# Kernel tuning notes

Measured on AMD Instinct MI355X. Metric: run time of the kernel, lower is better.

## Reference

```python
import jax, jax.numpy as jnp
import numpy as np

H = 16  # num_heads
B, N, M, D = 4, 512, 2048, 1024
FF = 4096  # mlp_ratio * D
LN_EPS = 1e-5


def _ln(x, g, b):
    m = x.mean(-1, keepdims=True)
    v = ((x - m) ** 2).mean(-1, keepdims=True)
    return (x - m) * jax.lax.rsqrt(v + LN_EPS) * g + b


def _attn(q_in, k_in, v_in, wq, bq, wk, bk, wv, bv, wp, bp):
    b, n, d = q_in.shape
    m = k_in.shape[1]
    hd = d // H
    scale = hd ** -0.5
    q = (q_in @ wq + bq).reshape(b, n, H, hd) * scale
    k = (k_in @ wk + bk).reshape(b, m, H, hd)
    v = (v_in @ wv + bv).reshape(b, m, H, hd)
    attn = jax.nn.softmax(jnp.einsum('bnhd,bmhd->bhnm', q, k), axis=-1)
    out = jnp.einsum('bhnm,bmhd->bnhd', attn, v).reshape(b, n, d)
    return out @ wp + bp


def setup_inputs() -> dict:
    key = jax.random.key(0)
    ks = iter(jax.random.split(key, 32))
    rnd = lambda shape: jax.random.normal(next(ks), shape, dtype=jnp.float32)
    w = lambda *shape: rnd(shape) * 0.02
    inp = {
        'state': rnd((B, N, D)),
        'patches': rnd((B, M, D)),
        'patches_pos_embed': rnd((B, M, D)),
        'state_query': rnd((B, N, D)),
    }
    for p in ('ca', 'sa'):
        inp[f'{p}_wq'] = w(D, D); inp[f'{p}_bq'] = jnp.zeros((D,), jnp.float32)
        inp[f'{p}_wk'] = w(D, D); inp[f'{p}_bk'] = jnp.zeros((D,), jnp.float32)
        inp[f'{p}_wv'] = w(D, D); inp[f'{p}_bv'] = jnp.zeros((D,), jnp.float32)
        inp[f'{p}_wp'] = w(D, D); inp[f'{p}_bp'] = jnp.zeros((D,), jnp.float32)
    inp['w1'] = w(D, FF); inp['b1'] = jnp.zeros((FF,), jnp.float32)
    inp['w2'] = w(FF, D); inp['b2'] = jnp.zeros((D,), jnp.float32)
    for i in (1, 2, 3):
        inp[f'n{i}_g'] = jnp.ones((D,), jnp.float32)
        inp[f'n{i}_b'] = jnp.zeros((D,), jnp.float32)
        inp[f'ls{i}'] = jnp.full((D,), 1e-5, jnp.float32)
    return inp


def reference(state, patches, patches_pos_embed, state_query,
              ca_wq, ca_bq, ca_wk, ca_bk, ca_wv, ca_bv, ca_wp, ca_bp,
              sa_wq, sa_bq, sa_wk, sa_bk, sa_wv, sa_bv, sa_wp, sa_bp,
              w1, b1, w2, b2,
              n1_g, n1_b, n2_g, n2_b, n3_g, n3_b,
              ls1, ls2, ls3):
    # pre-norm path of TransformerLayer.forward_pre (dropouts/drop_path = 0)
    state = state + state_query
    kv = patches + patches_pos_embed
    cross = _attn(_ln(state, n1_g, n1_b), kv, patches,
                  ca_wq, ca_bq, ca_wk, ca_bk, ca_wv, ca_bv, ca_wp, ca_bp)
    state = state + cross * ls1
    ns = _ln(state, n2_g, n2_b)
    selfa = _attn(ns, ns, ns,
                  sa_wq, sa_bq, sa_wk, sa_bk, sa_wv, sa_bv, sa_wp, sa_bp)
    state = state + selfa * ls2
    h = jax.nn.gelu(_ln(state, n3_g, n3_b) @ w1 + b1)
    return state + (h @ w2 + b2) * ls3
```

## Files before the change

### kernel.cpp

```cpp
#include <hip/hip_runtime.h>

#define DEV __device__ __forceinline__

typedef __bf16 bf16x8 __attribute__((ext_vector_type(8)));
typedef float f32x4 __attribute__((ext_vector_type(4)));

DEV unsigned short f2bf(float f) {
  __bf16 h = (__bf16)f;
  return __builtin_bit_cast(unsigned short, h);
}
DEV unsigned int cvtpk(float lo, float hi) {
  unsigned int r;
  asm("v_cvt_pk_bf16_f32 %0, %1, %2" : "=v"(r) : "v"(lo), "v"(hi));
  return r;
}

DEV void gload16(const void* g, void* l) {
  __builtin_amdgcn_global_load_lds(
      (const __attribute__((address_space(1))) unsigned int*)g,
      (__attribute__((address_space(3))) unsigned int*)l, 16, 0, 0);
}

DEV float gelu(float v) {
  const float u = 0.7978845608028654f * (v + 0.044715f * v * v * v);
  const float e = exp2f(u * 2.885390081777927f);
  return 0.5f * v * (2.f - 2.f / (e + 1.f));
}

DEV void tconv64_body(const float* __restrict__ W, unsigned short* __restrict__ Wt,
                      int K, int N, int bx, int by, float* tile ) {
  const int t = threadIdx.x;
  const int rr = t >> 4;
  const int cc = (t & 15) * 4;
#pragma unroll
  for (int it = 0; it < 4; it++) {
    float4 v = *reinterpret_cast<const float4*>(
        &W[(size_t)(by * 64 + it * 16 + rr) * N + bx * 64 + cc]);
    tile[(it * 16 + rr) * 65 + cc] = v.x;
    tile[(it * 16 + rr) * 65 + cc + 1] = v.y;
    tile[(it * 16 + rr) * 65 + cc + 2] = v.z;
    tile[(it * 16 + rr) * 65 + cc + 3] = v.w;
  }
  __syncthreads();
  const int nr = t >> 3;
  const int kc = (t & 7) * 8;
#pragma unroll
  for (int it = 0; it < 2; it++) {
    const int n = it * 32 + nr;
    uint4 o;
    o.x = cvtpk(tile[(kc + 0) * 65 + n], tile[(kc + 1) * 65 + n]);
    o.y = cvtpk(tile[(kc + 2) * 65 + n], tile[(kc + 3) * 65 + n]);
    o.z = cvtpk(tile[(kc + 4) * 65 + n], tile[(kc + 5) * 65 + n]);
    o.w = cvtpk(tile[(kc + 6) * 65 + n], tile[(kc + 7) * 65 + n]);
    *reinterpret_cast<uint4*>(&Wt[(size_t)(bx * 64 + n) * K + by * 64 + kc]) = o;
  }
}

DEV void add_ln_body(const float* __restrict__ a, const float* b, float* x0_out,
                     unsigned short* __restrict__ y, const float* __restrict__ gam,
                     const float* __restrict__ bet, int row) {
  const int t = threadIdx.x;
  const int c = t * 4;
  const size_t base = (size_t)row * 1024 + c;
  float4 v = *reinterpret_cast<const float4*>(a + base);
  if (b) {
    float4 v2 = *reinterpret_cast<const float4*>(b + base);
    v.x += v2.x; v.y += v2.y; v.z += v2.z; v.w += v2.w;
  }
  if (x0_out) *reinterpret_cast<float4*>(x0_out + base) = v;
  float s = v.x + v.y + v.z + v.w;
  float sq = v.x * v.x + v.y * v.y + v.z * v.z + v.w * v.w;
#pragma unroll
  for (int o = 32; o > 0; o >>= 1) {
    s += __shfl_xor(s, o);
    sq += __shfl_xor(sq, o);
  }
  __shared__ float ps[4], pq[4];
  const int w = t >> 6;
  if ((t & 63) == 0) { ps[w] = s; pq[w] = sq; }
  __syncthreads();
  s = ps[0] + ps[1] + ps[2] + ps[3];
  sq = pq[0] + pq[1] + pq[2] + pq[3];
  const float mean = s * (1.f / 1024.f);
  const float var = sq * (1.f / 1024.f) - mean * mean;
  const float rstd = rsqrtf(var + 1e-5f);
  float4 gv = *reinterpret_cast<const float4*>(gam + c);
  float4 bv = *reinterpret_cast<const float4*>(bet + c);
  uint2 o2;
  o2.x = cvtpk((v.x - mean) * rstd * gv.x + bv.x, (v.y - mean) * rstd * gv.y + bv.y);
  o2.y = cvtpk((v.z - mean) * rstd * gv.z + bv.z, (v.w - mean) * rstd * gv.w + bv.w);
  *reinterpret_cast<uint2*>(y + base) = o2;
}

DEV void kvcast_body8(const float* __restrict__ p, const float* __restrict__ pe,
                      unsigned short* __restrict__ kvo, unsigned short* __restrict__ po,
                      int bid) {
  const size_t i = ((size_t)bid * 256 + threadIdx.x) * 8;
  float4 a0 = *reinterpret_cast<const float4*>(p + i);
  float4 a1 = *reinterpret_cast<const float4*>(p + i + 4);
  float4 b0 = *reinterpret_cast<const float4*>(pe + i);
  float4 b1 = *reinterpret_cast<const float4*>(pe + i + 4);
  uint4 kv, pp;
  kv.x = cvtpk(a0.x + b0.x, a0.y + b0.y);
  kv.y = cvtpk(a0.z + b0.z, a0.w + b0.w);
  kv.z = cvtpk(a1.x + b1.x, a1.y + b1.y);
  kv.w = cvtpk(a1.z + b1.z, a1.w + b1.w);
  pp.x = cvtpk(a0.x, a0.y);
  pp.y = cvtpk(a0.z, a0.w);
  pp.z = cvtpk(a1.x, a1.y);
  pp.w = cvtpk(a1.z, a1.w);
  *reinterpret_cast<uint4*>(kvo + i) = kv;
  *reinterpret_cast<uint4*>(po + i) = pp;
}

struct Pre {
  const float* caw[3]; unsigned short* cad[3];
  const float* state; const float* squery; float* stateF; unsigned short* lnB;
  const float* n1_g; const float* n1_b;
  const float* patches; const float* ppe; unsigned short* kvB; unsigned short* patB;
};
__global__ __launch_bounds__(256) void prelude_kernel(Pre p) {
  __shared__ __align__(16) float tile[64 * 65];
  const int bid = blockIdx.x;
  if (bid < 4096) {
    kvcast_body8(p.patches, p.ppe, p.kvB, p.patB, bid);
  } else if (bid < 4864) {
    const int i = bid - 4096;
    const int m = i >> 8, wi = i & 255;
    tconv64_body(p.caw[m], p.cad[m], 1024, 1024, wi & 15, wi >> 4, tile);
  } else {
    add_ln_body(p.state, p.squery, p.stateF, p.lnB, p.n1_g, p.n1_b, bid - 4864);
  }
}

__global__ __launch_bounds__(256) void add_ln_kernel(
    const float* __restrict__ a, const float* b, float* x0_out,
    unsigned short* __restrict__ y, const float* __restrict__ gam,
    const float* __restrict__ bet) {
  add_ln_body(a, b, x0_out, y, gam, bet, blockIdx.x);
}

DEV void xcd_swizzle(int gx, int gy, int& bx, int& by, int& bz) {
  const int gxy = gx * gy;
  const int nwg = gxy * gridDim.z;
  const int orig = (blockIdx.z * gy + blockIdx.y) * gx + blockIdx.x;
  const int q = nwg >> 3, r = nwg & 7;
  const int xcd = orig & 7;
  int wgid = (xcd < r ? xcd * (q + 1) : r * (q + 1) + (xcd - r) * q) + (orig >> 3);
  bz = wgid / gxy;
  wgid -= bz * gxy;
  if (gy >= gx) { by = wgid / gx; bx = wgid - by * gx; }
  else          { bx = wgid / gy; by = wgid - bx * gy; }
}

template <int BM, int BN>
DEV void gemm_core(const unsigned short* __restrict__ A,
                   const unsigned short* __restrict__ Bt,
                   unsigned short* As, unsigned short* Bs,
                   int brow, int bcol, int K, int lda, int koff,
                   f32x4 (&acc)[BM / 32][BN / 32]) {
  constexpr int WM = BM / 32, WN = BN / 32;
  const int t = threadIdx.x;
  const int lane = t & 63, w = t >> 6;
  const int wr = w >> 1, wc = w & 1;
  const int g = lane >> 4, lr = lane & 15;
  const int srow = lane >> 2, scol = (lane & 3) * 8;

  auto stage = [&](int buf, int k0) {
#pragma unroll
    for (int i = 0; i < BM / 64; i++) {
      const int r0 = (i * 4 + w) * 16;
      gload16(A + (size_t)(brow + r0 + srow) * lda + koff + k0 + scol,
              &As[buf * BM * 32 + r0 * 32]);
    }
#pragma unroll
    for (int i = 0; i < BN / 64; i++) {
      const int r0 = (i * 4 + w) * 16;
      gload16(Bt + (size_t)(bcol + r0 + srow) * lda + koff + k0 + scol,
              &Bs[buf * BN * 32 + r0 * 32]);
    }
  };

  stage(0, 0);
  const int nk = K / 32;
  int cur = 0;
  for (int kt = 0; kt < nk; kt++) {
    __syncthreads();
    if (kt + 1 < nk) stage(cur ^ 1, (kt + 1) * 32);
    bf16x8 af[WM], bfr[WN];
#pragma unroll
    for (int m = 0; m < WM; m++)
      af[m] = *reinterpret_cast<const bf16x8*>(
          &As[cur * BM * 32 + (wr * (BM / 2) + m * 16 + lr) * 32 + g * 8]);
#pragma unroll
    for (int n = 0; n < WN; n++)
      bfr[n] = *reinterpret_cast<const bf16x8*>(
          &Bs[cur * BN * 32 + (wc * (BN / 2) + n * 16 + lr) * 32 + g * 8]);
    __builtin_amdgcn_s_setprio(1);
#pragma unroll
    for (int m = 0; m < WM; m++)
#pragma unroll
      for (int n = 0; n < WN; n++)
        acc[m][n] = __builtin_amdgcn_mfma_f32_16x16x32_bf16(af[m], bfr[n], acc[m][n], 0, 0, 0);
    __builtin_amdgcn_s_setprio(0);
    cur ^= 1;
  }
}

template <int BM, int BN>
DEV void epilogue_vT(f32x4 (&acc)[BM / 32][BN / 32], unsigned short* smem,
                     unsigned short* __restrict__ vT, const float* __restrict__ bias,
                     int brow, int bcol, int vcol0, int vNk, int rpb) {
  constexpr int WM = BM / 32, WN = BN / 32;
  constexpr int LDT = 136;
  const int t = threadIdx.x, lane = t & 63, w = t >> 6;
  const int wr = w >> 1, wc = w & 1;
  const int g = lane >> 4, lr = lane & 15;
  __syncthreads();
#pragma unroll
  for (int m = 0; m < WM; m++) {
    const int row0 = wr * (BM / 2) + m * 16 + g * 4;
#pragma unroll
    for (int n = 0; n < WN; n++) {
      const int cc = wc * (BN / 2) + n * 16 + lr;
      const float bv = bias[bcol + cc];
      uint2 pk;
      pk.x = cvtpk(acc[m][n][0] + bv, acc[m][n][1] + bv);
      pk.y = cvtpk(acc[m][n][2] + bv, acc[m][n][3] + bv);
      *reinterpret_cast<uint2*>(&smem[cc * LDT + row0]) = pk;
    }
  }
  __syncthreads();
  const int b = brow / rpb;
  const int kvb = brow % rpb;
  constexpr int ITERS = BM * BN / (256 * 8);
#pragma unroll
  for (int it = 0; it < ITERS; it++) {
    const int idx = it * 256 + t;
    const int cc = idx / (BM / 8);
    const int ch = idx % (BM / 8);
    const int dg = bcol + cc - vcol0;
    const int h = dg >> 6, d = dg & 63;
    uint4 v = *reinterpret_cast<uint4*>(&smem[cc * LDT + ch * 8]);
    *reinterpret_cast<uint4*>(
        &vT[((size_t)(b * 16 + h) * 64 + d) * vNk + kvb + ch * 8]) = v;
  }
}

template <int EPI, int BM, int BN>
__global__ __launch_bounds__(256) void gemm_kernel(
    const unsigned short* __restrict__ A, const unsigned short* __restrict__ Bt,
    const float* __restrict__ bias, const float* resid,
    const float* __restrict__ ls, void* outp, int M, int N, int K, int lda) {
  constexpr int WM = BM / 32;
  constexpr int WN = BN / 32;
  __shared__ __align__(16) unsigned short smem[2 * BM * 32 + 2 * BN * 32];
  unsigned short* As = smem;
  unsigned short* Bs = smem + 2 * BM * 32;
  const int t = threadIdx.x;
  const int lane = t & 63, w = t >> 6;
  const int wr = w >> 1, wc = w & 1;
  const int g = lane >> 4, lr = lane & 15;

  int bx, by, bz;
  xcd_swizzle(gridDim.x, gridDim.y, bx, by, bz);
  const int brow = by * BM, bcol = bx * BN;

  f32x4 acc[WM][WN] = {};
  gemm_core<BM, BN>(A, Bt, As, Bs, brow, bcol, K, lda, bz * K, acc);

#pragma unroll
  for (int m = 0; m < WM; m++) {
    const int row0 = brow + wr * (BM / 2) + m * 16 + g * 4;
#pragma unroll
    for (int n = 0; n < WN; n++) {
      const int col = bcol + wc * (BN / 2) + n * 16 + lr;
      const float bv = (EPI == 4) ? 0.f : bias[col];
#pragma unroll
      for (int r = 0; r < 4; r++) {
        const float v = acc[m][n][r] + bv;
        const size_t idx = (size_t)(row0 + r) * N + col;
        if (EPI == 0) {
          ((unsigned short*)outp)[idx] = f2bf(v);
        } else if (EPI == 2) {
          ((float*)outp)[idx] = resid[idx] + v * ls[col];
        } else if (EPI == 3) {
          ((unsigned short*)outp)[idx] = f2bf(gelu(v));
        } else {
          ((float*)outp)[(size_t)bz * M * N + idx] = v;
        }
      }
    }
  }
}

struct G3X {
  const unsigned short* A[3]; const unsigned short* Bt[3];
  const float* bias[3]; unsigned short* out[3]; int ecum[3];
  unsigned short* vT; int vNk; int rpb;
  const float* wp; unsigned short* wpt;
  const float* saw[4]; unsigned short* sad[4];
  const float* bq; const float* bk; const float* bv; float* bqkv;
};
__global__ __launch_bounds__(256) void gemm3_kernel(G3X p, int N, int K) {
  constexpr int BM = 128, BN = 128, WM = BM / 32, WN = BN / 32;
  constexpr int STG = 2 * BM * 32 + 2 * BN * 32;
  constexpr int TRN = BN * 136;
  constexpr int SME = (TRN > STG) ? TRN : STG;
  constexpr int NG = 1152;
  __shared__ __align__(16) unsigned short smem[SME];
  const int bid = blockIdx.x;
  const int t = threadIdx.x;

  if (bid >= NG) {
    float* tile = reinterpret_cast<float*>(smem);
    int i = bid - NG;
    if (i < 256) {
      tconv64_body(p.wp, p.wpt, 1024, 1024, i & 15, i >> 4, tile);
    } else if (i < 1280) {
      i -= 256;
      const int m = i >> 8, wi = i & 255;
      tconv64_body(p.saw[m], p.sad[m], 1024, 1024, wi & 15, wi >> 4, tile);
    } else {
      const int j = (i - 1280) * 256 + t;
      p.bqkv[j] = j < 1024 ? p.bq[j] : (j < 2048 ? p.bk[j - 1024] : p.bv[j - 2048]);
    }
    return;
  }

  unsigned short* As = smem;
  unsigned short* Bs = smem + 2 * BM * 32;
  const int lane = t & 63, w = t >> 6;
  const int wr = w >> 1, wc = w & 1;
  const int g = lane >> 4, lr = lane & 15;
  const int wgid = (bid & 7) * (NG >> 3) + (bid >> 3);
  const int by = wgid >> 3, bx = wgid & 7;
  const int s = (by >= p.ecum[0]) + (by >= p.ecum[1]);
  const int byloc = by - (s ? p.ecum[s - 1] : 0);
  const unsigned short* A = p.A[s];
  const unsigned short* Bt = p.Bt[s];
  const float* bias = p.bias[s];
  const int brow = byloc * BM, bcol = bx * BN;

  f32x4 acc[WM][WN] = {};
  gemm_core<BM, BN>(A, Bt, As, Bs, brow, bcol, K, K, 0, acc);

  if (s == 2) {
    epilogue_vT<BM, BN>(acc, smem, p.vT, bias, brow, bcol, 0, p.vNk, p.rpb);
    return;
  }
  unsigned short* outp = p.out[s];
#pragma unroll
  for (int m = 0; m < WM; m++) {
    const int row0 = brow + wr * (BM / 2) + m * 16 + g * 4;
#pragma unroll
    for (int n = 0; n < WN; n++) {
      const int col = bcol + wc * (BN / 2) + n * 16 + lr;
      const float bv = bias[col];
#pragma unroll
      for (int r = 0; r < 4; r++)
        outp[(size_t)(row0 + r) * N + col] = f2bf(acc[m][n][r] + bv);
    }
  }
}

struct G5X {
  const unsigned short* A; const unsigned short* Bt;
  const float* bias; unsigned short* out;
  unsigned short* vT; int vcol0; int vNk; int rpb;
  const float* w1; unsigned short* w1t;
  const float* w2; unsigned short* w2t;
};
__global__ __launch_bounds__(256) void gemm5x_kernel(G5X p, int M, int N, int K) {
  constexpr int BM = 128, BN = 64, WM = BM / 32, WN = BN / 32;
  constexpr int STG = 2 * BM * 32 + 2 * BN * 32;
  __shared__ __align__(16) unsigned short smem[STG];
  constexpr int NG = 768;
  const int bid = blockIdx.x;
  const int t = threadIdx.x;

  if (bid >= NG) {
    float* tile = reinterpret_cast<float*>(smem);
    int i = bid - NG;
    if (i < 1024) {
      tconv64_body(p.w1, p.w1t, 1024, 4096, i & 63, i >> 6, tile);
    } else {
      i -= 1024;
      tconv64_body(p.w2, p.w2t, 4096, 1024, i & 15, i >> 4, tile);
    }
    return;
  }

  unsigned short* As = smem;
  unsigned short* Bs = smem + 2 * BM * 32;
  const int lane = t & 63, w = t >> 6;
  const int wr = w >> 1, wc = w & 1;
  const int g = lane >> 4, lr = lane & 15;
  const int wgid = (bid & 7) * (NG >> 3) + (bid >> 3);
  const int bx = wgid >> 4, by = wgid & 15;
  const int brow = by * BM, bcol = bx * BN;

  f32x4 acc[WM][WN] = {};
  gemm_core<BM, BN>(p.A, p.Bt, As, Bs, brow, bcol, K, K, 0, acc);

  if (bcol >= p.vcol0) {
    epilogue_vT<BM, BN>(acc, smem, p.vT, p.bias, brow, bcol, p.vcol0, p.vNk, p.rpb);
    return;
  }
#pragma unroll
  for (int m = 0; m < WM; m++) {
    const int row0 = brow + wr * (BM / 2) + m * 16 + g * 4;
#pragma unroll
    for (int n = 0; n < WN; n++) {
      const int col = bcol + wc * (BN / 2) + n * 16 + lr;
      const float bv = p.bias[col];
#pragma unroll
      for (int r = 0; r < 4; r++)
        p.out[(size_t)(row0 + r) * N + col] = f2bf(acc[m][n][r] + bv);
    }
  }
}

__global__ __launch_bounds__(256) void splitk_red_kernel(
    const float* __restrict__ p, const float* __restrict__ bias,
    const float* __restrict__ resid, const float* __restrict__ ls,
    float* __restrict__ out) {
  const size_t i = ((size_t)blockIdx.x * 256 + threadIdx.x) * 4;
  const int c = (int)(i & 1023);
  float4 a = *reinterpret_cast<const float4*>(p + i);
  float4 b = *reinterpret_cast<const float4*>(p + 2048ull * 1024 + i);
  float4 rv = *reinterpret_cast<const float4*>(resid + i);
  float4 bb = *reinterpret_cast<const float4*>(bias + c);
  float4 lv = *reinterpret_cast<const float4*>(ls + c);
  float4 o;
  o.x = rv.x + (a.x + b.x + bb.x) * lv.x;
  o.y = rv.y + (a.y + b.y + bb.y) * lv.y;
  o.z = rv.z + (a.z + b.z + bb.z) * lv.z;
  o.w = rv.w + (a.w + b.w + bb.w) * lv.w;
  *reinterpret_cast<float4*>(out + i) = o;
}

__global__ __launch_bounds__(512) void attn_kernel(
    const unsigned short* __restrict__ Q, const unsigned short* __restrict__ Kp,
    const unsigned short* __restrict__ vT, unsigned short* __restrict__ O,
    int RSq, int RSk, int Nq, int Nk, float k2) {
  __shared__ __align__(16) unsigned short Ks[2][128 * 72];
  __shared__ __align__(16) unsigned short Vs[2][64 * 136];
  __shared__ __align__(16) unsigned short Ps[128 * 136];
  const int t = threadIdx.x, lane = t & 63, w = t >> 6;
  const int qt = blockIdx.y, h = blockIdx.x & 15, b = blockIdx.x >> 4;
  const int g = lane >> 4, lr = lane & 15;
  const int ksrow = t >> 2, kscol = (t & 3) * 16;
  const int vsrow = t >> 3, vscol = (t & 7) * 16;

  uint4 qr[2];
  {
    const unsigned short* qp = Q + (size_t)(b * Nq + qt * 128 + w * 16 + lr) * RSq + h * 64 + g * 8;
    qr[0] = *reinterpret_cast<const uint4*>(qp);
    qr[1] = *reinterpret_cast<const uint4*>(qp + 32);
  }
  float m_i = -1e30f, l_i = 0.f;
  f32x4 acc_o[4] = {};

  auto kaddr = [&](int kv0) {
    return reinterpret_cast<const uint4*>(
        Kp + (size_t)(b * Nk + kv0 + ksrow) * RSk + h * 64 + kscol);
  };
  auto vaddr = [&](int kv0) {
    return reinterpret_cast<const uint4*>(
        vT + ((size_t)(b * 16 + h) * 64 + vsrow) * Nk + kv0 + vscol);
  };

  uint4 kr0 = kaddr(0)[0], kr1 = kaddr(0)[1];
  uint4 vr0 = vaddr(0)[0], vr1 = vaddr(0)[1];

  int cur = 0;
  for (int kv0 = 0; kv0 < Nk; kv0 += 128) {
    *reinterpret_cast<uint4*>(&Ks[cur][ksrow * 72 + kscol]) = kr0;
    *reinterpret_cast<uint4*>(&Ks[cur][ksrow * 72 + kscol + 8]) = kr1;
    *reinterpret_cast<uint4*>(&Vs[cur][vsrow * 136 + vscol]) = vr0;
    *reinterpret_cast<uint4*>(&Vs[cur][vsrow * 136 + vscol + 8]) = vr1;
    __syncthreads();
    if (kv0 + 128 < Nk) {
      kr0 = kaddr(kv0 + 128)[0]; kr1 = kaddr(kv0 + 128)[1];
      vr0 = vaddr(kv0 + 128)[0]; vr1 = vaddr(kv0 + 128)[1];
    }

    f32x4 accs[8] = {};
    __builtin_amdgcn_s_setprio(1);
#pragma unroll
    for (int d0 = 0; d0 < 64; d0 += 32) {
      bf16x8 qf = __builtin_bit_cast(bf16x8, qr[d0 >> 5]);
#pragma unroll
      for (int m = 0; m < 8; m++) {
        bf16x8 kf = *reinterpret_cast<const bf16x8*>(&Ks[cur][(m * 16 + lr) * 72 + d0 + g * 8]);
        accs[m] = __builtin_amdgcn_mfma_f32_16x16x32_bf16(kf, qf, accs[m], 0, 0, 0);
      }
    }
    __builtin_amdgcn_s_setprio(0);
    float pmax = -1e30f;
#pragma unroll
    for (int m = 0; m < 8; m++)
#pragma unroll
      for (int r = 0; r < 4; r++) pmax = fmaxf(pmax, accs[m][r]);
    pmax = fmaxf(pmax, __shfl_xor(pmax, 16));
    pmax = fmaxf(pmax, __shfl_xor(pmax, 32));
    const float pm2 = pmax * k2;
    if (!__all(pm2 <= m_i + 8.f)) {
      const float m_new = fmaxf(m_i, pm2);
      const float corr = exp2f(m_i - m_new);
      m_i = m_new;
      l_i *= corr;
#pragma unroll
      for (int r = 0; r < 4; r++) {
        const float cf = __shfl(corr, g * 4 + r);
#pragma unroll
        for (int n = 0; n < 4; n++) acc_o[n][r] *= cf;
      }
    }
    float psum = 0.f;
#pragma unroll
    for (int m = 0; m < 8; m++) {
      float p0 = exp2f(fmaf(accs[m][0], k2, -m_i));
      float p1 = exp2f(fmaf(accs[m][1], k2, -m_i));
      float p2 = exp2f(fmaf(accs[m][2], k2, -m_i));
      float p3 = exp2f(fmaf(accs[m][3], k2, -m_i));
      psum += p0 + p1 + p2 + p3;
      uint2 pk;
      pk.x = cvtpk(p0, p1);
      pk.y = cvtpk(p2, p3);
      *reinterpret_cast<uint2*>(&Ps[(w * 16 + lr) * 136 + m * 16 + g * 4]) = pk;
    }
    psum += __shfl_xor(psum, 16);
    psum += __shfl_xor(psum, 32);
    l_i += psum;
    __builtin_amdgcn_s_setprio(1);
#pragma unroll
    for (int ks = 0; ks < 4; ks++) {
      bf16x8 pf = *reinterpret_cast<const bf16x8*>(&Ps[(w * 16 + lr) * 136 + ks * 32 + g * 8]);
#pragma unroll
      for (int n = 0; n < 4; n++) {
        bf16x8 vf = *reinterpret_cast<const bf16x8*>(&Vs[cur][(n * 16 + lr) * 136 + ks * 32 + g * 8]);
        acc_o[n] = __builtin_amdgcn_mfma_f32_16x16x32_bf16(pf, vf, acc_o[n], 0, 0, 0);
      }
    }
    __builtin_amdgcn_s_setprio(0);
    cur ^= 1;
  }
#pragma unroll
  for (int r = 0; r < 4; r++) {
    const float li = __shfl(l_i, g * 4 + r);
    const float inv = 1.f / li;
    const int qrow = qt * 128 + w * 16 + g * 4 + r;
#pragma unroll
    for (int n = 0; n < 4; n++)
      O[(size_t)(b * Nq + qrow) * 1024 + h * 64 + n * 16 + lr] = f2bf(acc_o[n][r] * inv);
  }
}

extern "C" void kernel_launch(void* const* d_in, const int* in_sizes, int n_in,
                              void* d_out, int out_size, void* d_ws, size_t ws_size,
                              hipStream_t stream) {
  const float* state = (const float*)d_in[0];
  const float* patches = (const float*)d_in[1];
  const float* ppe = (const float*)d_in[2];
  const float* squery = (const float*)d_in[3];
  const float* ca_wq = (const float*)d_in[4];
  const float* ca_bq = (const float*)d_in[5];
  const float* ca_wk = (const float*)d_in[6];
  const float* ca_bk = (const float*)d_in[7];
  const float* ca_wv = (const float*)d_in[8];
  const float* ca_bv = (const float*)d_in[9];
  const float* ca_wp = (const float*)d_in[10];
  const float* ca_bp = (const float*)d_in[11];
  const float* sa_wq = (const float*)d_in[12];
  const float* sa_bq = (const float*)d_in[13];
  const float* sa_wk = (const float*)d_in[14];
  const float* sa_bk = (const float*)d_in[15];
  const float* sa_wv = (const float*)d_in[16];
  const float* sa_bv = (const float*)d_in[17];
  const float* sa_wp = (const float*)d_in[18];
  const float* sa_bp = (const float*)d_in[19];
  const float* w1 = (const float*)d_in[20];
  const float* b1 = (const float*)d_in[21];
  const float* w2 = (const float*)d_in[22];
  const float* b2 = (const float*)d_in[23];
  const float* n1_g = (const float*)d_in[24];
  const float* n1_b = (const float*)d_in[25];
  const float* ls1 = (const float*)d_in[26];
  const float* n2_g = (const float*)d_in[27];
  const float* n2_b = (const float*)d_in[28];
  const float* ls2 = (const float*)d_in[29];
  const float* n3_g = (const float*)d_in[30];
  const float* n3_b = (const float*)d_in[31];
  const float* ls3 = (const float*)d_in[32];

  char* wsp = (char*)d_ws;
  auto alloc = [&](size_t bytes) {
    void* p = (void*)wsp;
    wsp += (bytes + 255) & ~(size_t)255;
    return p;
  };
  float* stateF = (float*)alloc(2048ull * 1024 * 4);
  unsigned short* lnB = (unsigned short*)alloc(2048ull * 1024 * 2);
  unsigned short* kvB = (unsigned short*)alloc(8192ull * 1024 * 2);
  unsigned short* patB = (unsigned short*)alloc(8192ull * 1024 * 2);
  unsigned short* qB = (unsigned short*)alloc(2048ull * 1024 * 2);
  unsigned short* kB = (unsigned short*)alloc(8192ull * 1024 * 2);
  unsigned short* vB = (unsigned short*)alloc(8192ull * 1024 * 2);
  unsigned short* oB = (unsigned short*)alloc(2048ull * 1024 * 2);
  unsigned short* hB = kvB;
  unsigned short* qkvB = kB;
  unsigned short* vTc = vB;
  unsigned short* vTs = qB;
  float* mlp2p = (float*)patB;
  unsigned short* ca_wqt = (unsigned short*)alloc(1024ull * 1024 * 2);
  unsigned short* ca_wkt = (unsigned short*)alloc(1024ull * 1024 * 2);
  unsigned short* ca_wvt = (unsigned short*)alloc(1024ull * 1024 * 2);
  unsigned short* ca_wpt = (unsigned short*)alloc(1024ull * 1024 * 2);
  unsigned short* sa_wqkvt = (unsigned short*)alloc(3072ull * 1024 * 2);
  unsigned short* sa_wpt = (unsigned short*)alloc(1024ull * 1024 * 2);
  unsigned short* w1t = (unsigned short*)alloc(4096ull * 1024 * 2);
  unsigned short* w2t = (unsigned short*)alloc(4096ull * 1024 * 2);
  float* sa_bqkv = (float*)alloc(3072 * 4);

  Pre pre;
  pre.caw[0] = ca_wq; pre.cad[0] = ca_wqt;
  pre.caw[1] = ca_wk; pre.cad[1] = ca_wkt;
  pre.caw[2] = ca_wv; pre.cad[2] = ca_wvt;
  pre.state = state; pre.squery = squery; pre.stateF = stateF; pre.lnB = lnB;
  pre.n1_g = n1_g; pre.n1_b = n1_b;
  pre.patches = patches; pre.ppe = ppe; pre.kvB = kvB; pre.patB = patB;
  prelude_kernel<<<6912, 256, 0, stream>>>(pre);

  const float k2 = 0.125f * 1.4426950408889634f;

  G3X g3;
  g3.A[0] = lnB;  g3.Bt[0] = ca_wqt; g3.bias[0] = ca_bq; g3.out[0] = qB;      g3.ecum[0] = 16;
  g3.A[1] = kvB;  g3.Bt[1] = ca_wkt; g3.bias[1] = ca_bk; g3.out[1] = kB;      g3.ecum[1] = 80;
  g3.A[2] = patB; g3.Bt[2] = ca_wvt; g3.bias[2] = ca_bv; g3.out[2] = nullptr; g3.ecum[2] = 144;
  g3.vT = vTc; g3.vNk = 2048; g3.rpb = 2048;
  g3.wp = ca_wp; g3.wpt = ca_wpt;
  g3.saw[0] = sa_wq; g3.sad[0] = sa_wqkvt;
  g3.saw[1] = sa_wk; g3.sad[1] = sa_wqkvt + 1024ull * 1024;
  g3.saw[2] = sa_wv; g3.sad[2] = sa_wqkvt + 2048ull * 1024;
  g3.saw[3] = sa_wp; g3.sad[3] = sa_wpt;
  g3.bq = sa_bq; g3.bk = sa_bk; g3.bv = sa_bv; g3.bqkv = sa_bqkv;
  gemm3_kernel<<<2444, 256, 0, stream>>>(g3, 1024, 1024);
  attn_kernel<<<dim3(64, 4), 512, 0, stream>>>(qB, kB, vTc, oB, 1024, 1024, 512, 2048, k2);
  gemm_kernel<2, 64, 64><<<dim3(16, 32), 256, 0, stream>>>(oB, ca_wpt, ca_bp, stateF, ls1, stateF, 2048, 1024, 1024, 1024);

  add_ln_kernel<<<2048, 256, 0, stream>>>(stateF, nullptr, nullptr, lnB, n2_g, n2_b);
  G5X g5;
  g5.A = lnB; g5.Bt = sa_wqkvt; g5.bias = sa_bqkv; g5.out = qkvB;
  g5.vT = vTs; g5.vcol0 = 2048; g5.vNk = 512; g5.rpb = 512;
  g5.w1 = w1; g5.w1t = w1t; g5.w2 = w2; g5.w2t = w2t;
  gemm5x_kernel<<<2816, 256, 0, stream>>>(g5, 2048, 3072, 1024);
  attn_kernel<<<dim3(64, 4), 512, 0, stream>>>(qkvB, qkvB + 1024, vTs, oB, 3072, 3072, 512, 512, k2);
  gemm_kernel<2, 64, 64><<<dim3(16, 32), 256, 0, stream>>>(oB, sa_wpt, sa_bp, stateF, ls2, stateF, 2048, 1024, 1024, 1024);

  add_ln_kernel<<<2048, 256, 0, stream>>>(stateF, nullptr, nullptr, lnB, n3_g, n3_b);
  gemm_kernel<3, 128, 128><<<dim3(32, 16), 256, 0, stream>>>(lnB, w1t, b1, nullptr, nullptr, hB, 2048, 4096, 1024, 1024);
  gemm_kernel<4, 128, 64><<<dim3(16, 16, 2), 256, 0, stream>>>(hB, w2t, nullptr, nullptr, nullptr, mlp2p, 2048, 1024, 2048, 4096);
  splitk_red_kernel<<<2048, 256, 0, stream>>>(mlp2p, b2, stateF, ls3, (float*)d_out);
}
```

Measured before the change: 277.7 us.

## Split cross-attention over KV into two chunks with combine kernel, single-buffer LDS

Cross-attention (2048 keys) is now split along the key dimension into two grid z-slices. Each slice writes unnormalized fp32 partial outputs plus running max and sum, and a new combine kernel merges them into bf16 output. The goal is to double the block count (256 to 512 blocks) so more CUs are busy. LDS K/V tiles drop from double to single buffering with an extra barrier per iteration, which cuts shared memory use but serializes tile stores against compute. In exchange the change adds an extra kernel launch and fp32 partial-result traffic.

Measured after the change: 278.5 us. Within noise of the previous version (+0.3%).

```diff
diff --git a/kernel.cpp b/kernel.cpp
--- a/kernel.cpp
+++ b/kernel.cpp
@@ -440,15 +440,19 @@
   *reinterpret_cast<float4*>(out + i) = o;
 }
 
+template <int SPLIT>
 __global__ __launch_bounds__(512) void attn_kernel(
     const unsigned short* __restrict__ Q, const unsigned short* __restrict__ Kp,
     const unsigned short* __restrict__ vT, unsigned short* __restrict__ O,
-    int RSq, int RSk, int Nq, int Nk, float k2) {
-  __shared__ __align__(16) unsigned short Ks[2][128 * 72];
-  __shared__ __align__(16) unsigned short Vs[2][64 * 136];
+    float* __restrict__ opart, float* __restrict__ mlbuf,
+    int RSq, int RSk, int Nq, int NkTot, int NkL, float k2) {
+  __shared__ __align__(16) unsigned short Ks[128 * 72];
+  __shared__ __align__(16) unsigned short Vs[64 * 136];
   __shared__ __align__(16) unsigned short Ps[128 * 136];
   const int t = threadIdx.x, lane = t & 63, w = t >> 6;
   const int qt = blockIdx.y, h = blockIdx.x & 15, b = blockIdx.x >> 4;
+  const int z = blockIdx.z;
+  const int kvbase = z * NkL;
   const int g = lane >> 4, lr = lane & 15;
   const int ksrow = t >> 2, kscol = (t & 3) * 16;
   const int vsrow = t >> 3, vscol = (t & 7) * 16;
@@ -464,24 +468,23 @@
 
   auto kaddr = [&](int kv0) {
     return reinterpret_cast<const uint4*>(
-        Kp + (size_t)(b * Nk + kv0 + ksrow) * RSk + h * 64 + kscol);
+        Kp + (size_t)(b * NkTot + kvbase + kv0 + ksrow) * RSk + h * 64 + kscol);
   };
   auto vaddr = [&](int kv0) {
     return reinterpret_cast<const uint4*>(
-        vT + ((size_t)(b * 16 + h) * 64 + vsrow) * Nk + kv0 + vscol);
+        vT + ((size_t)(b * 16 + h) * 64 + vsrow) * NkTot + kvbase + kv0 + vscol);
   };
 
   uint4 kr0 = kaddr(0)[0], kr1 = kaddr(0)[1];
   uint4 vr0 = vaddr(0)[0], vr1 = vaddr(0)[1];
 
-  int cur = 0;
-  for (int kv0 = 0; kv0 < Nk; kv0 += 128) {
-    *reinterpret_cast<uint4*>(&Ks[cur][ksrow * 72 + kscol]) = kr0;
-    *reinterpret_cast<uint4*>(&Ks[cur][ksrow * 72 + kscol + 8]) = kr1;
-    *reinterpret_cast<uint4*>(&Vs[cur][vsrow * 136 + vscol]) = vr0;
-    *reinterpret_cast<uint4*>(&Vs[cur][vsrow * 136 + vscol + 8]) = vr1;
+  for (int kv0 = 0; kv0 < NkL; kv0 += 128) {
+    *reinterpret_cast<uint4*>(&Ks[ksrow * 72 + kscol]) = kr0;
+    *reinterpret_cast<uint4*>(&Ks[ksrow * 72 + kscol + 8]) = kr1;
+    *reinterpret_cast<uint4*>(&Vs[vsrow * 136 + vscol]) = vr0;
+    *reinterpret_cast<uint4*>(&Vs[vsrow * 136 + vscol + 8]) = vr1;
     __syncthreads();
-    if (kv0 + 128 < Nk) {
+    if (kv0 + 128 < NkL) {
       kr0 = kaddr(kv0 + 128)[0]; kr1 = kaddr(kv0 + 128)[1];
       vr0 = vaddr(kv0 + 128)[0]; vr1 = vaddr(kv0 + 128)[1];
     }
@@ -493,7 +496,7 @@
       bf16x8 qf = __builtin_bit_cast(bf16x8, qr[d0 >> 5]);
 #pragma unroll
       for (int m = 0; m < 8; m++) {
-        bf16x8 kf = *reinterpret_cast<const bf16x8*>(&Ks[cur][(m * 16 + lr) * 72 + d0 + g * 8]);
+        bf16x8 kf = *reinterpret_cast<const bf16x8*>(&Ks[(m * 16 + lr) * 72 + d0 + g * 8]);
         accs[m] = __builtin_amdgcn_mfma_f32_16x16x32_bf16(kf, qf, accs[m], 0, 0, 0);
       }
     }
@@ -540,22 +543,58 @@
       bf16x8 pf = *reinterpret_cast<const bf16x8*>(&Ps[(w * 16 + lr) * 136 + ks * 32 + g * 8]);
 #pragma unroll
       for (int n = 0; n < 4; n++) {
-        bf16x8 vf = *reinterpret_cast<const bf16x8*>(&Vs[cur][(n * 16 + lr) * 136 + ks * 32 + g * 8]);
+        bf16x8 vf = *reinterpret_cast<const bf16x8*>(&Vs[(n * 16 + lr) * 136 + ks * 32 + g * 8]);
         acc_o[n] = __builtin_amdgcn_mfma_f32_16x16x32_bf16(pf, vf, acc_o[n], 0, 0, 0);
       }
     }
     __builtin_amdgcn_s_setprio(0);
-    cur ^= 1;
-  }
-#pragma unroll
-  for (int r = 0; r < 4; r++) {
-    const float li = __shfl(l_i, g * 4 + r);
-    const float inv = 1.f / li;
-    const int qrow = qt * 128 + w * 16 + g * 4 + r;
-#pragma unroll
-    for (int n = 0; n < 4; n++)
-      O[(size_t)(b * Nq + qrow) * 1024 + h * 64 + n * 16 + lr] = f2bf(acc_o[n][r] * inv);
-  }
+    __syncthreads();
+  }
+
+  if (SPLIT) {
+    const int R0 = ((b * 16 + h) << 9) + qt * 128 + w * 16;
+    if (lane < 16) {
+      mlbuf[(size_t)(R0 + lr) * 4 + z * 2] = m_i;
+      mlbuf[(size_t)(R0 + lr) * 4 + z * 2 + 1] = l_i;
+    }
+#pragma unroll
+    for (int r = 0; r < 4; r++) {
+      const int R = R0 + g * 4 + r;
+#pragma unroll
+      for (int n = 0; n < 4; n++)
+        opart[((size_t)z * 32768 + R) * 64 + n * 16 + lr] = acc_o[n][r];
+    }
+  } else {
+#pragma unroll
+    for (int r = 0; r < 4; r++) {
+      const float li = __shfl(l_i, g * 4 + r);
+      const float inv = 1.f / li;
+      const int qrow = qt * 128 + w * 16 + g * 4 + r;
+#pragma unroll
+      for (int n = 0; n < 4; n++)
+        O[(size_t)(b * Nq + qrow) * 1024 + h * 64 + n * 16 + lr] = f2bf(acc_o[n][r] * inv);
+    }
+  }
+}
+
+__global__ __launch_bounds__(256) void attn_combine_kernel(
+    const float* __restrict__ opart, const float* __restrict__ mlbuf,
+    unsigned short* __restrict__ O) {
+  const int idx = blockIdx.x * 256 + threadIdx.x;
+  const int R = idx >> 4;
+  const int dq = (idx & 15) * 4;
+  const float m1 = mlbuf[R * 4 + 0], l1 = mlbuf[R * 4 + 1];
+  const float m2 = mlbuf[R * 4 + 2], l2 = mlbuf[R * 4 + 3];
+  const float mm = fmaxf(m1, m2);
+  const float e1 = exp2f(m1 - mm), e2 = exp2f(m2 - mm);
+  const float inv = 1.f / (e1 * l1 + e2 * l2);
+  float4 a = *reinterpret_cast<const float4*>(&opart[(size_t)R * 64 + dq]);
+  float4 b = *reinterpret_cast<const float4*>(&opart[(size_t)(R + 32768) * 64 + dq]);
+  const int bb = R >> 13, h = (R >> 9) & 15, q = R & 511;
+  uint2 pk;
+  pk.x = cvtpk((e1 * a.x + e2 * b.x) * inv, (e1 * a.y + e2 * b.y) * inv);
+  pk.y = cvtpk((e1 * a.z + e2 * b.z) * inv, (e1 * a.w + e2 * b.w) * inv);
+  *reinterpret_cast<uint2*>(O + ((size_t)(bb * 512 + q)) * 1024 + h * 64 + dq) = pk;
 }
 
 extern "C" void kernel_launch(void* const* d_in, const int* in_sizes, int n_in,
@@ -613,6 +652,7 @@
   unsigned short* qkvB = kB;
   unsigned short* vTc = vB;
   unsigned short* vTs = qB;
+  float* opart = (float*)patB;
   float* mlp2p = (float*)patB;
   unsigned short* ca_wqt = (unsigned short*)alloc(1024ull * 1024 * 2);
   unsigned short* ca_wkt = (unsigned short*)alloc(1024ull * 1024 * 2);
@@ -623,6 +663,7 @@
   unsigned short* w1t = (unsigned short*)alloc(4096ull * 1024 * 2);
   unsigned short* w2t = (unsigned short*)alloc(4096ull * 1024 * 2);
   float* sa_bqkv = (float*)alloc(3072 * 4);
+  float* mlbuf = (float*)alloc(32768ull * 4 * 4);
 
   Pre pre;
   pre.caw[0] = ca_wq; pre.cad[0] = ca_wqt;
@@ -647,7 +688,9 @@
   g3.saw[3] = sa_wp; g3.sad[3] = sa_wpt;
   g3.bq = sa_bq; g3.bk = sa_bk; g3.bv = sa_bv; g3.bqkv = sa_bqkv;
   gemm3_kernel<<<2444, 256, 0, stream>>>(g3, 1024, 1024);
-  attn_kernel<<<dim3(64, 4), 512, 0, stream>>>(qB, kB, vTc, oB, 1024, 1024, 512, 2048, k2);
+  attn_kernel<1><<<dim3(64, 4, 2), 512, 0, stream>>>(
+      qB, kB, vTc, nullptr, opart, mlbuf, 1024, 1024, 512, 2048, 1024, k2);
+  attn_combine_kernel<<<2048, 256, 0, stream>>>(opart, mlbuf, oB);
   gemm_kernel<2, 64, 64><<<dim3(16, 32), 256, 0, stream>>>(oB, ca_wpt, ca_bp, stateF, ls1, stateF, 2048, 1024, 1024, 1024);
 
   add_ln_kernel<<<2048, 256, 0, stream>>>(stateF, nullptr, nullptr, lnB, n2_g, n2_b);
@@ -656,7 +699,8 @@
   g5.vT = vTs; g5.vcol0 = 2048; g5.vNk = 512; g5.rpb = 512;
   g5.w1 = w1; g5.w1t = w1t; g5.w2 = w2; g5.w2t = w2t;
   gemm5x_kernel<<<2816, 256, 0, stream>>>(g5, 2048, 3072, 1024);
-  attn_kernel<<<dim3(64, 4), 512, 0, stream>>>(qkvB, qkvB + 1024, vTs, oB, 3072, 3072, 512, 512, k2);
+  attn_kernel<0><<<dim3(64, 4, 1), 512, 0, stream>>>(
+      qkvB, qkvB + 1024, vTs, oB, nullptr, nullptr, 3072, 3072, 512, 512, 512, k2);
   gemm_kernel<2, 64, 64><<<dim3(16, 32), 256, 0, stream>>>(oB, sa_wpt, sa_bp, stateF, ls2, stateF, 2048, 1024, 1024, 1024);
 
   add_ln_kernel<<<2048, 256, 0, stream>>>(stateF, nullptr, nullptr, lnB, n3_g, n3_b);
```
